# Optimization experiments

Measured on AMD Instinct MI355X. Metric: run time of the kernel, lower is better.

Reference implementation:

```python
import jax, jax.numpy as jnp
import numpy as np
from jax import lax

B, C_IN, C_OUT, H, W, K = 32, 128, 256, 56, 56, 3
STRIDE, PAD = 1, 1
LAMBDA_C, LAMBDA_A = 0.0, 1.0  # adaptive_weights=False defaults


def setup_inputs() -> dict:
    key = jax.random.key(0)
    k1, k2, k3 = jax.random.split(key, 3)
    x = jax.random.normal(k1, (B, C_IN, H, W), dtype=jnp.float32)
    weight = jax.random.normal(k2, (C_OUT, C_IN, K, K), dtype=jnp.float32) * 0.05
    bias = jax.random.normal(k3, (C_OUT,), dtype=jnp.float32) * 0.05
    return {"x": x, "weight": weight, "bias": bias}


def reference(x, weight, bias):
    # For each k x k patch X and kernel slice Kc (per in-channel):
    #   sum(X@Kc) = sum_{a,c} X[a,c] * rowsum(Kc)[c]   (depends on patch column index)
    #   sum(Kc@X) = sum_{c,b} X[c,b] * colsum(Kc)[c]   (depends on patch row index)
    # So lambda_c*(XK-KX).sum() + lambda_a*(XK+KX).sum() summed over in-channels is
    # exactly a conv2d with the effective kernel below.
    krow = weight.sum(axis=3)  # [O, I, k]  rowsum: sum over last kernel axis
    kcol = weight.sum(axis=2)  # [O, I, k]  colsum: sum over first kernel axis
    # W_eff[o,i,r,s] = (la+lc)*krow[o,i,s] + (la-lc)*kcol[o,i,r]
    w_eff = (LAMBDA_A + LAMBDA_C) * krow[:, :, None, :] \
          + (LAMBDA_A - LAMBDA_C) * kcol[:, :, :, None]
    y = lax.conv_general_dilated(
        x, w_eff,
        window_strides=(STRIDE, STRIDE),
        padding=[(PAD, PAD), (PAD, PAD)],
        dimension_numbers=("NCHW", "OIHW", "NCHW"),
    )
    return y + bias[None, :, None, None]
```

## Files before the change

kernel.cpp:

```cpp
#include <hip/hip_runtime.h>
#include <hip/hip_fp16.h>
#include <stdint.h>

typedef unsigned short u16;
typedef _Float16 half8 __attribute__((ext_vector_type(8)));
typedef float floatx4 __attribute__((ext_vector_type(4)));

#define B_N 32
#define CI  128
#define CO  256
#define HH  56
#define WW  56
#define HP  58
#define WP  58

static const size_t XP_OFF = 590080;
static const size_t XP_SZ  = (size_t)32 * 58 * 7424 * 2;
static const size_t XV_OFF = XP_OFF + XP_SZ;
static const size_t XV_SZ  = (size_t)32 * 56 * 7424 * 2;
static const size_t XH_OFF = XV_OFF + XV_SZ;
static const size_t XH_SZ  = (size_t)32 * 58 * 7168 * 2;
static const size_t WS_NEED = XH_OFF + XH_SZ + 1024;

__device__ __forceinline__ float bf2f(u16 u) {
  union { uint32_t i; float f; } c; c.i = ((uint32_t)u) << 16; return c.f;
}
__device__ __forceinline__ u16 f2bf(float f) {
  union { float f; uint32_t i; } c; c.f = f;
  uint32_t u = c.i;
  u += 0x7fffu + ((u >> 16) & 1u);
  return (u16)(u >> 16);
}
__device__ __forceinline__ u16 f2h16(float f) {
  __half h = __float2half_rn(f);
  return *reinterpret_cast<u16*>(&h);
}
__device__ __forceinline__ uint32_t pack2h(float a, float b) {
  __half2 h = __floats2half2_rn(a, b);
  return *reinterpret_cast<uint32_t*>(&h);
}
__device__ __forceinline__ int4 add3(int4 a, int4 b, int4 c) {
  __half2* pa = (__half2*)&a; __half2* pb = (__half2*)&b; __half2* pc = (__half2*)&c;
  int4 r; __half2* pr = (__half2*)&r;
#pragma unroll
  for (int i = 0; i < 4; ++i) pr[i] = __hadd2(__hadd2(pa[i], pb[i]), pc[i]);
  return r;
}

__device__ __forceinline__ bool detect_bf16(const void* __restrict__ bias) {
  int lane = threadIdx.x & 63;
  float a = fabsf(bf2f(((const u16*)bias)[lane]));
  bool plausible = (a >= 1e-5f) && (a <= 0.5f);
  unsigned long long m = __ballot(plausible);
  return __popcll(m) >= 50;
}

__global__ __launch_bounds__(256) void k_prep(const void* __restrict__ xsrc,
                                              const void* __restrict__ wsrc,
                                              u16* __restrict__ xp,
                                              u16* __restrict__ wb,
                                              const void* __restrict__ bias) {
  const int hp = blockIdx.x, b = blockIdx.y, tid = threadIdx.x;
  if (hp == HP) {
    const bool isbf = detect_bf16(bias);
#pragma unroll 1
    for (int sub = 0; sub < 4; ++sub) {
      int t = (b * 4 + sub) * 256 + tid;
      float v[9];
      if (isbf) {
        const u16* p = (const u16*)wsrc + (size_t)t * 9;
#pragma unroll
        for (int j = 0; j < 9; ++j) v[j] = bf2f(p[j]);
      } else {
        const float* p = (const float*)wsrc + (size_t)t * 9;
#pragma unroll
        for (int j = 0; j < 9; ++j) v[j] = p[j];
      }
      float rowsum[3] = { v[0]+v[1]+v[2], v[3]+v[4]+v[5], v[6]+v[7]+v[8] };
      float colsum[3] = { v[0]+v[3]+v[6], v[1]+v[4]+v[7], v[2]+v[5]+v[8] };
      const int o = t >> 7, i = t & 127;
      const int osub = o >> 4, lo = o & 15;
      const int ic = i >> 5, q = (i >> 3) & 3, j = i & 7;
#pragma unroll
      for (int s = 0; s < 3; ++s) {
        int k = s * 4 + ic;
        wb[((size_t)(k * 16 + osub) * 64 + q * 16 + lo) * 8 + j] = f2h16(rowsum[s]);
      }
#pragma unroll
      for (int r = 0; r < 3; ++r) {
        int k = 12 + r * 4 + ic;
        wb[((size_t)(k * 16 + osub) * 64 + q * 16 + lo) * 8 + j] = f2h16(colsum[r]);
      }
    }
    return;
  }
  __shared__ uint32_t tile32[CI * 29];
  u16* dst = xp + (size_t)(b * HP + hp) * (16 * WP * 8);
  if (hp == 0 || hp == HP - 1) {
    int4 z = {0, 0, 0, 0};
    for (int c = tid; c < 928; c += 256) *(int4*)(dst + c * 8) = z;
    return;
  }
  const bool isbf = detect_bf16(bias);
  const int h = hp - 1;
  if (isbf) {
    const uint32_t* xr = (const uint32_t*)xsrc;
    for (int c = tid; c < CI * 28; c += 256) {
      int i = c / 28, wp = c - i * 28;
      uint32_t p2 = xr[((size_t)(b * CI + i) * HH + h) * 28 + wp];
      tile32[i * 29 + wp] = pack2h(bf2f((u16)p2), bf2f((u16)(p2 >> 16)));
    }
  } else {
    const float4* xr = (const float4*)xsrc;
    for (int c = tid; c < CI * 14; c += 256) {
      int i = c / 14, f4 = c - i * 14;
      float4 v = xr[((size_t)(b * CI + i) * HH + h) * 14 + f4];
      tile32[i * 29 + 2 * f4]     = pack2h(v.x, v.y);
      tile32[i * 29 + 2 * f4 + 1] = pack2h(v.z, v.w);
    }
  }
  __syncthreads();
  const u16* t16 = (const u16*)tile32;
  uint32_t* dw = (uint32_t*)dst;
  for (int c = tid; c < 16 * 56 * 4; c += 256) {
    int g = c / 224, rem = c - g * 224, w = rem >> 2, jj = rem & 3;
    int i0 = g * 8 + jj * 2;
    uint32_t lo16 = t16[i0 * 58 + w], hi16 = t16[(i0 + 1) * 58 + w];
    dw[(g * 58 + (w + 1)) * 4 + jj] = lo16 | (hi16 << 16);
  }
  if (tid < 128) {
    int g = tid >> 3, k = tid & 7, wb_ = (k >> 2) * 57, jj = k & 3;
    dw[(g * 58 + wb_) * 4 + jj] = 0;
  }
}

__global__ __launch_bounds__(256) void k_box(const u16* __restrict__ xp,
                                             u16* __restrict__ xv,
                                             u16* __restrict__ xh) {
  const int u = blockIdx.x, b = blockIdx.y, tid = threadIdx.x;
  const int4* r0 = (const int4*)(xp + (size_t)(b * HP + u) * 7424);
  int4* hd = (int4*)(xh + (size_t)(b * HP + u) * 7168);
  for (int c = tid; c < 16 * 56; c += 256) {
    int g = c / 56, w = c - g * 56;
    const int4* s = r0 + g * 58 + w;
    hd[c] = add3(s[0], s[1], s[2]);
  }
  if (u < HH) {
    int4* vd = (int4*)(xv + (size_t)(b * HH + u) * 7424);
    const int4 *r1 = r0 + 928, *r2 = r0 + 1856;
    for (int c = tid; c < 928; c += 256) vd[c] = add3(r0[c], r1[c], r2[c]);
  }
}

#define GSTRIDE 472
#define RSTRIDE (16 * 472)

#define ALOAD(BUF, K)                                                       \
  {                                                                         \
    const u16* ap = wb + ((size_t)((K)*16 + osubbase) << 9) + lane * 8;     \
    af[BUF][0] = *(const half8*)ap;                                         \
    af[BUF][1] = *(const half8*)(ap + 512);                                 \
    af[BUF][2] = *(const half8*)(ap + 1024);                                \
    af[BUF][3] = *(const half8*)(ap + 1536);                                \
  }
#define BLOAD(BUF, K)                                                       \
  {                                                                         \
    int ic_ = (K)&3;                                                        \
    int t_, co_;                                                            \
    if ((K) < 12) { t_ = 2 * rp;                    co_ = (lo + ((K) >> 2)) * 8; } \
    else          { t_ = 4 + 2 * rp + (((K)-12) >> 2); co_ = lo * 8; }      \
    const u16* bp = Bs + ((t_ * 16 + ic_ * 4 + quad) * GSTRIDE) + co_;      \
    bfr[BUF][0] = *(const half8*)bp;                                        \
    bfr[BUF][1] = *(const half8*)(bp + 128);                                \
    bfr[BUF][2] = *(const half8*)(bp + 256);                                \
    bfr[BUF][3] = *(const half8*)(bp + 384);                                \
    bfr[BUF][4] = *(const half8*)(bp + RSTRIDE);                            \
    bfr[BUF][5] = *(const half8*)(bp + RSTRIDE + 128);                      \
    bfr[BUF][6] = *(const half8*)(bp + RSTRIDE + 256);                      \
    bfr[BUF][7] = *(const half8*)(bp + RSTRIDE + 384);                      \
  }
#define MSTEP(BUF)                                                          \
  _Pragma("unroll") for (int m = 0; m < 4; ++m)                             \
      _Pragma("unroll") for (int n = 0; n < 8; ++n) acc[m][n] =             \
          __builtin_amdgcn_mfma_f32_16x16x32_f16(af[BUF][m], bfr[BUF][n],   \
                                                 acc[m][n], 0, 0, 0);

__global__ __launch_bounds__(512, 2) void k_gemm(const u16* __restrict__ wb,
                                                 const u16* __restrict__ xp,
                                                 const void* __restrict__ bias,
                                                 void* __restrict__ outv) {
  __shared__ u16 Bs[10 * RSTRIDE + 64];
  const int lin = blockIdx.y * (HH / 4) + blockIdx.x;
  const int swz = (lin & 7) * (448 / 8) + (lin >> 3);
  const int b = swz / (HH / 4);
  const int p0 = 4 * (swz - b * (HH / 4));
  const int tid = threadIdx.x;
  const int wv = tid >> 6, lane = tid & 63;
  const int lo = lane & 15, quad = lane >> 4;
  const int aq = wv & 3, rp = wv >> 2;
  const int osubbase = aq * 4;

  {
    const u16* xb = xp + (size_t)(b * HP) * 7424;
    for (int c = tid; c < 4 * 928; c += 512) {
      int t = c / 928, rem = c - t * 928;
      const int4* src = (const int4*)(xb + (size_t)(p0 + t) * 7424) + rem;
      int g = rem / 58, w = rem - g * 58;
      *(int4*)(Bs + (size_t)((t * 16 + g) * 59 + w) * 8) =
          add3(src[0], src[928], src[1856]);
    }
    for (int c = tid; c < 6 * 896; c += 512) {
      int u = c / 896, rem = c - u * 896;
      int g = rem / 56, w = rem - g * 56;
      const int4* src = (const int4*)(xb + (size_t)(p0 + u) * 7424) + g * 58 + w;
      *(int4*)(Bs + (size_t)(((4 + u) * 16 + g) * 59 + w) * 8) =
          add3(src[0], src[1], src[2]);
    }
    if (tid < 192) {
      int u = tid / 32, rem = tid - u * 32, g = rem >> 1, w = 56 + (rem & 1);
      *(int4*)(Bs + (size_t)(((4 + u) * 16 + g) * 59 + w) * 8) = (int4){0, 0, 0, 0};
    }
  }
  __syncthreads();

  floatx4 acc[4][8];
#pragma unroll
  for (int m = 0; m < 4; ++m)
#pragma unroll
    for (int n = 0; n < 8; ++n) acc[m][n] = (floatx4){0.f, 0.f, 0.f, 0.f};

  half8 af[2][4], bfr[2][8];
  ALOAD(0, 0); BLOAD(0, 0);
#pragma unroll 1
  for (int k = 0; k < 24; k += 2) {
    ALOAD(1, k + 1); BLOAD(1, k + 1);
    MSTEP(0);
    if (k + 2 < 24) { ALOAD(0, k + 2); BLOAD(0, k + 2); }
    MSTEP(1);
  }

  const bool isbf = detect_bf16(bias);
  const int prow = p0 + 2 * rp;
  if (isbf) {
    u16* out = (u16*)outv;
    const u16* bs = (const u16*)bias;
#pragma unroll
    for (int m = 0; m < 4; ++m)
#pragma unroll
      for (int v = 0; v < 4; ++v) {
        const int o = aq * 64 + m * 16 + quad * 4 + v;
        const float bv = bf2f(bs[o]);
        size_t base = ((size_t)(b * CO + o) * HH + prow) * WW;
#pragma unroll
        for (int n = 0; n < 8; ++n) {
          const int q = (n & 3) * 16 + lo;
          if (q < WW) out[base + (n >> 2) * WW + q] = f2bf(acc[m][n][v] + bv);
        }
      }
  } else {
    float* out = (float*)outv;
    const float* bs = (const float*)bias;
#pragma unroll
    for (int m = 0; m < 4; ++m)
#pragma unroll
      for (int v = 0; v < 4; ++v) {
        const int o = aq * 64 + m * 16 + quad * 4 + v;
        const float bv = bs[o];
        size_t base = ((size_t)(b * CO + o) * HH + prow) * WW;
#pragma unroll
        for (int n = 0; n < 8; ++n) {
          const int q = (n & 3) * 16 + lo;
          if (q < WW) out[base + (n >> 2) * WW + q] = acc[m][n][v] + bv;
        }
      }
  }
}

#define ALOAD_D(BUF, K)                                                     \
  {                                                                         \
    const u16* ap = wb + ((size_t)((K)*16 + osubbase) << 9) + lane * 8;     \
    af[BUF][0] = *(const half8*)ap;                                         \
    af[BUF][1] = *(const half8*)(ap + 512);                                 \
    af[BUF][2] = *(const half8*)(ap + 1024);                                \
    af[BUF][3] = *(const half8*)(ap + 1536);                                \
  }
#define BLOAD_D(BUF, K)                                                     \
  {                                                                         \
    const int g_ = ((K)&3) * 4 + quad;                                      \
    const u16* bp; size_t rstr;                                             \
    if ((K) < 12) {                                                         \
      bp = xv + ((size_t)((b * HH + p0) * 16 + g_)) * 464 + (lo + ((K) >> 2)) * 8; \
      rstr = 7424;                                                          \
    } else {                                                                \
      bp = xh + ((size_t)((b * HP + p0 + (((K)-12) >> 2)) * 16 + g_)) * 448 + lo * 8; \
      rstr = 7168;                                                          \
    }                                                                       \
    bfr[BUF][0] = *(const half8*)bp;                                        \
    bfr[BUF][1] = *(const half8*)(bp + 128);                                \
    bfr[BUF][2] = *(const half8*)(bp + 256);                                \
    bfr[BUF][3] = *(const half8*)(bp + 384);                                \
    bfr[BUF][4] = *(const half8*)(bp + rstr);                               \
    bfr[BUF][5] = *(const half8*)(bp + rstr + 128);                         \
    bfr[BUF][6] = *(const half8*)(bp + rstr + 256);                         \
    bfr[BUF][7] = *(const half8*)(bp + rstr + 384);                         \
  }

__global__ __launch_bounds__(256, 2) void k_gemm_d(const u16* __restrict__ wb,
                                                   const u16* __restrict__ xv,
                                                   const u16* __restrict__ xh,
                                                   const void* __restrict__ bias,
                                                   void* __restrict__ outv) {
  const int lin = blockIdx.y * (HH / 2) + blockIdx.x;
  const int swz = (lin & 7) * 112 + (lin >> 3);
  const int b = swz / (HH / 2);
  const int p0 = 2 * (swz - b * (HH / 2));
  const int tid = threadIdx.x;
  const int wv = tid >> 6, lane = tid & 63;
  const int lo = lane & 15, quad = lane >> 4;
  const int osubbase = wv * 4;

  floatx4 acc[4][8];
#pragma unroll
  for (int m = 0; m < 4; ++m)
#pragma unroll
    for (int n = 0; n < 8; ++n) acc[m][n] = (floatx4){0.f, 0.f, 0.f, 0.f};

  half8 af[2][4], bfr[2][8];
  ALOAD_D(0, 0); BLOAD_D(0, 0);
#pragma unroll 1
  for (int k = 0; k < 24; k += 2) {
    ALOAD_D(1, k + 1); BLOAD_D(1, k + 1);
    MSTEP(0);
    if (k + 2 < 24) { ALOAD_D(0, k + 2); BLOAD_D(0, k + 2); }
    MSTEP(1);
  }

  const bool isbf = detect_bf16(bias);
  if (isbf) {
    u16* out = (u16*)outv;
    const u16* bs = (const u16*)bias;
#pragma unroll
    for (int m = 0; m < 4; ++m)
#pragma unroll
      for (int v = 0; v < 4; ++v) {
        const int o = wv * 64 + m * 16 + quad * 4 + v;
        const float bv = bf2f(bs[o]);
        size_t base = ((size_t)(b * CO + o) * HH + p0) * WW;
#pragma unroll
        for (int n = 0; n < 8; ++n) {
          const int q = (n & 3) * 16 + lo;
          if (q < WW) out[base + (n >> 2) * WW + q] = f2bf(acc[m][n][v] + bv);
        }
      }
  } else {
    float* out = (float*)outv;
    const float* bs = (const float*)bias;
#pragma unroll
    for (int m = 0; m < 4; ++m)
#pragma unroll
      for (int v = 0; v < 4; ++v) {
        const int o = wv * 64 + m * 16 + quad * 4 + v;
        const float bv = bs[o];
        size_t base = ((size_t)(b * CO + o) * HH + p0) * WW;
#pragma unroll
        for (int n = 0; n < 8; ++n) {
          const int q = (n & 3) * 16 + lo;
          if (q < WW) out[base + (n >> 2) * WW + q] = acc[m][n][v] + bv;
        }
      }
  }
}

extern "C" void kernel_launch(void* const* d_in, const int* in_sizes, int n_in,
                              void* d_out, int out_size, void* d_ws, size_t ws_size,
                              hipStream_t stream) {
  const void* x    = d_in[0];
  const void* w    = d_in[1];
  const void* bias = d_in[2];
  uint8_t* ws = (uint8_t*)d_ws;
  u16* wb = (u16*)ws;
  u16* xp = (u16*)(ws + XP_OFF);

  k_prep<<<dim3(HP + 1, B_N), 256, 0, stream>>>(x, w, xp, wb, bias);
  if (ws_size >= WS_NEED) {
    u16* xv = (u16*)(ws + XV_OFF);
    u16* xh = (u16*)(ws + XH_OFF);
    k_box<<<dim3(HP, B_N), 256, 0, stream>>>(xp, xv, xh);
    k_gemm_d<<<dim3(HH / 2, B_N), 256, 0, stream>>>(wb, xv, xh, bias, d_out);
  } else {
    k_gemm<<<dim3(HH / 4, B_N), 512, 0, stream>>>(wb, xp, bias, d_out);
  }
}
```

Before: 222.5 us.

## Fuse vertical box-sum into GEMM via shared memory, drop xv buffer

Stops writing the vertically summed tensor xv to global memory in the box kernel. The GEMM kernel now computes the vertical 3-row sums for its two output rows directly from the padded input and stages them in shared memory, then reads B fragments from LDS for the first 12 k-steps. The horizontal-sum path still reads xh from global memory. This removes one large global write and read pass, at the cost of extra LDS use and a sync at kernel start.

Result: faster. 204.1 us (-8.3%).

```diff
diff --git a/kernel.cpp b/kernel.cpp
--- a/kernel.cpp
+++ b/kernel.cpp
@@ -135,7 +135,6 @@
 }
 
 __global__ __launch_bounds__(256) void k_box(const u16* __restrict__ xp,
-                                             u16* __restrict__ xv,
                                              u16* __restrict__ xh) {
   const int u = blockIdx.x, b = blockIdx.y, tid = threadIdx.x;
   const int4* r0 = (const int4*)(xp + (size_t)(b * HP + u) * 7424);
@@ -145,11 +144,6 @@
     const int4* s = r0 + g * 58 + w;
     hd[c] = add3(s[0], s[1], s[2]);
   }
-  if (u < HH) {
-    int4* vd = (int4*)(xv + (size_t)(b * HH + u) * 7424);
-    const int4 *r1 = r0 + 928, *r2 = r0 + 1856;
-    for (int c = tid; c < 928; c += 256) vd[c] = add3(r0[c], r1[c], r2[c]);
-  }
 }
 
 #define GSTRIDE 472
@@ -163,6 +157,12 @@
     af[BUF][2] = *(const half8*)(ap + 1024);                                \
     af[BUF][3] = *(const half8*)(ap + 1536);                                \
   }
+#define MSTEP(BUF)                                                          \
+  _Pragma("unroll") for (int m = 0; m < 4; ++m)                             \
+      _Pragma("unroll") for (int n = 0; n < 8; ++n) acc[m][n] =             \
+          __builtin_amdgcn_mfma_f32_16x16x32_f16(af[BUF][m], bfr[BUF][n],   \
+                                                 acc[m][n], 0, 0, 0);
+
 #define BLOAD(BUF, K)                                                       \
   {                                                                         \
     int ic_ = (K)&3;                                                        \
@@ -179,11 +179,6 @@
     bfr[BUF][6] = *(const half8*)(bp + RSTRIDE + 256);                      \
     bfr[BUF][7] = *(const half8*)(bp + RSTRIDE + 384);                      \
   }
-#define MSTEP(BUF)                                                          \
-  _Pragma("unroll") for (int m = 0; m < 4; ++m)                             \
-      _Pragma("unroll") for (int n = 0; n < 8; ++n) acc[m][n] =             \
-          __builtin_amdgcn_mfma_f32_16x16x32_f16(af[BUF][m], bfr[BUF][n],   \
-                                                 acc[m][n], 0, 0, 0);
 
 __global__ __launch_bounds__(512, 2) void k_gemm(const u16* __restrict__ wb,
                                                  const u16* __restrict__ xp,
@@ -276,23 +271,15 @@
   }
 }
 
-#define ALOAD_D(BUF, K)                                                     \
+#define BLOAD_H(BUF, K)                                                     \
   {                                                                         \
-    const u16* ap = wb + ((size_t)((K)*16 + osubbase) << 9) + lane * 8;     \
-    af[BUF][0] = *(const half8*)ap;                                         \
-    af[BUF][1] = *(const half8*)(ap + 512);                                 \
-    af[BUF][2] = *(const half8*)(ap + 1024);                                \
-    af[BUF][3] = *(const half8*)(ap + 1536);                                \
-  }
-#define BLOAD_D(BUF, K)                                                     \
-  {                                                                         \
-    const int g_ = ((K)&3) * 4 + quad;                                      \
+    const int ic_ = (K)&3;                                                  \
     const u16* bp; size_t rstr;                                             \
     if ((K) < 12) {                                                         \
-      bp = xv + ((size_t)((b * HH + p0) * 16 + g_)) * 464 + (lo + ((K) >> 2)) * 8; \
-      rstr = 7424;                                                          \
+      bp = Bs + ((ic_ * 4 + quad) * GSTRIDE) + (lo + ((K) >> 2)) * 8;       \
+      rstr = RSTRIDE;                                                       \
     } else {                                                                \
-      bp = xh + ((size_t)((b * HP + p0 + (((K)-12) >> 2)) * 16 + g_)) * 448 + lo * 8; \
+      bp = xh + ((size_t)((b * HP + p0 + (((K)-12) >> 2)) * 16 + ic_ * 4 + quad)) * 448 + lo * 8; \
       rstr = 7168;                                                          \
     }                                                                       \
     bfr[BUF][0] = *(const half8*)bp;                                        \
@@ -300,16 +287,17 @@
     bfr[BUF][2] = *(const half8*)(bp + 256);                                \
     bfr[BUF][3] = *(const half8*)(bp + 384);                                \
     bfr[BUF][4] = *(const half8*)(bp + rstr);                               \
-    bfr[BUF][5] = *(const half8*)(bp + rstr + 128);                         \
-    bfr[BUF][6] = *(const half8*)(bp + rstr + 256);                         \
-    bfr[BUF][7] = *(const half8*)(bp + rstr + 384);                         \
-  }
-
-__global__ __launch_bounds__(256, 2) void k_gemm_d(const u16* __restrict__ wb,
-                                                   const u16* __restrict__ xv,
+    bfr[BUF][5] = *(const half8*)(bp + rstr + 128);                        \
+    bfr[BUF][6] = *(const half8*)(bp + rstr + 256);                        \
+    bfr[BUF][7] = *(const half8*)(bp + rstr + 384);                        \
+  }
+
+__global__ __launch_bounds__(256, 2) void k_gemm_h(const u16* __restrict__ wb,
+                                                   const u16* __restrict__ xp,
                                                    const u16* __restrict__ xh,
                                                    const void* __restrict__ bias,
                                                    void* __restrict__ outv) {
+  __shared__ u16 Bs[2 * RSTRIDE + 64];
   const int lin = blockIdx.y * (HH / 2) + blockIdx.x;
   const int swz = (lin & 7) * 112 + (lin >> 3);
   const int b = swz / (HH / 2);
@@ -319,6 +307,20 @@
   const int lo = lane & 15, quad = lane >> 4;
   const int osubbase = wv * 4;
 
+  {
+    const u16* xb = xp + (size_t)(b * HP) * 7424;
+    for (int c = tid; c < 2 * 928; c += 256) {
+      int t = c >> 9 >= 1 ? c / 928 : 0;
+      t = c / 928;
+      int rem = c - t * 928;
+      const int4* src = (const int4*)(xb + (size_t)(p0 + t) * 7424) + rem;
+      int g = rem / 58, w = rem - g * 58;
+      *(int4*)(Bs + (size_t)((t * 16 + g) * 59 + w) * 8) =
+          add3(src[0], src[928], src[1856]);
+    }
+  }
+  __syncthreads();
+
   floatx4 acc[4][8];
 #pragma unroll
   for (int m = 0; m < 4; ++m)
@@ -326,12 +328,12 @@
     for (int n = 0; n < 8; ++n) acc[m][n] = (floatx4){0.f, 0.f, 0.f, 0.f};
 
   half8 af[2][4], bfr[2][8];
-  ALOAD_D(0, 0); BLOAD_D(0, 0);
+  ALOAD(0, 0); BLOAD_H(0, 0);
 #pragma unroll 1
   for (int k = 0; k < 24; k += 2) {
-    ALOAD_D(1, k + 1); BLOAD_D(1, k + 1);
+    ALOAD(1, k + 1); BLOAD_H(1, k + 1);
     MSTEP(0);
-    if (k + 2 < 24) { ALOAD_D(0, k + 2); BLOAD_D(0, k + 2); }
+    if (k + 2 < 24) { ALOAD(0, k + 2); BLOAD_H(0, k + 2); }
     MSTEP(1);
   }
 
@@ -383,10 +385,9 @@
 
   k_prep<<<dim3(HP + 1, B_N), 256, 0, stream>>>(x, w, xp, wb, bias);
   if (ws_size >= WS_NEED) {
-    u16* xv = (u16*)(ws + XV_OFF);
     u16* xh = (u16*)(ws + XH_OFF);
-    k_box<<<dim3(HP, B_N), 256, 0, stream>>>(xp, xv, xh);
-    k_gemm_d<<<dim3(HH / 2, B_N), 256, 0, stream>>>(wb, xv, xh, bias, d_out);
+    k_box<<<dim3(HP, B_N), 256, 0, stream>>>(xp, xh);
+    k_gemm_h<<<dim3(HH / 2, B_N), 256, 0, stream>>>(wb, xp, xh, bias, d_out);
   } else {
     k_gemm<<<dim3(HH / 4, B_N), 512, 0, stream>>>(wb, xp, bias, d_out);
   }
```

## Fuse box filtering into prep and GEMM, drop separate box kernel

Applied to the files above, without the earlier changes.

Removes the k_box kernel and the xv buffer. The horizontal 3-tap sum is now computed in k_prep from the shared-memory tile. The vertical 3-row sum is built inside the GEMM kernel into LDS from xp. The GEMM is restructured to one output row per block (4x4 MFMA tiles instead of 4x8) with occupancy hint 3, which cuts a launch and a global round trip. The cost is redundant vertical summing per block, less register reuse per block, and an LDS staging sync.

New measurement: 203.5 us. -8.5%, faster.

```diff
diff --git a/kernel.cpp b/kernel.cpp
--- a/kernel.cpp
+++ b/kernel.cpp
@@ -16,9 +16,7 @@
 
 static const size_t XP_OFF = 590080;
 static const size_t XP_SZ  = (size_t)32 * 58 * 7424 * 2;
-static const size_t XV_OFF = XP_OFF + XP_SZ;
-static const size_t XV_SZ  = (size_t)32 * 56 * 7424 * 2;
-static const size_t XH_OFF = XV_OFF + XV_SZ;
+static const size_t XH_OFF = XP_OFF + XP_SZ;
 static const size_t XH_SZ  = (size_t)32 * 58 * 7168 * 2;
 static const size_t WS_NEED = XH_OFF + XH_SZ + 1024;
 
@@ -58,8 +56,10 @@
 __global__ __launch_bounds__(256) void k_prep(const void* __restrict__ xsrc,
                                               const void* __restrict__ wsrc,
                                               u16* __restrict__ xp,
+                                              u16* __restrict__ xh,
                                               u16* __restrict__ wb,
-                                              const void* __restrict__ bias) {
+                                              const void* __restrict__ bias,
+                                              const int do_xh) {
   const int hp = blockIdx.x, b = blockIdx.y, tid = threadIdx.x;
   if (hp == HP) {
     const bool isbf = detect_bf16(bias);
@@ -95,14 +95,18 @@
     return;
   }
   __shared__ uint32_t tile32[CI * 29];
-  u16* dst = xp + (size_t)(b * HP + hp) * (16 * WP * 8);
+  u16* dst  = xp + (size_t)(b * HP + hp) * (16 * WP * 8);
+  u16* dsth = xh + (size_t)(b * HP + hp) * 7168;
   if (hp == 0 || hp == HP - 1) {
     int4 z = {0, 0, 0, 0};
     for (int c = tid; c < 928; c += 256) *(int4*)(dst + c * 8) = z;
+    if (do_xh)
+      for (int c = tid; c < 896; c += 256) *(int4*)(dsth + c * 8) = z;
     return;
   }
   const bool isbf = detect_bf16(bias);
   const int h = hp - 1;
+  if (tid < 128) tile32[tid * 29 + 28] = 0;
   if (isbf) {
     const uint32_t* xr = (const uint32_t*)xsrc;
     for (int c = tid; c < CI * 28; c += 256) {
@@ -132,23 +136,21 @@
     int g = tid >> 3, k = tid & 7, wb_ = (k >> 2) * 57, jj = k & 3;
     dw[(g * 58 + wb_) * 4 + jj] = 0;
   }
-}
-
-__global__ __launch_bounds__(256) void k_box(const u16* __restrict__ xp,
-                                             u16* __restrict__ xv,
-                                             u16* __restrict__ xh) {
-  const int u = blockIdx.x, b = blockIdx.y, tid = threadIdx.x;
-  const int4* r0 = (const int4*)(xp + (size_t)(b * HP + u) * 7424);
-  int4* hd = (int4*)(xh + (size_t)(b * HP + u) * 7168);
-  for (int c = tid; c < 16 * 56; c += 256) {
-    int g = c / 56, w = c - g * 56;
-    const int4* s = r0 + g * 58 + w;
-    hd[c] = add3(s[0], s[1], s[2]);
-  }
-  if (u < HH) {
-    int4* vd = (int4*)(xv + (size_t)(b * HH + u) * 7424);
-    const int4 *r1 = r0 + 928, *r2 = r0 + 1856;
-    for (int c = tid; c < 928; c += 256) vd[c] = add3(r0[c], r1[c], r2[c]);
+  if (do_xh) {
+    const __half* ha = (const __half*)t16;
+    uint32_t* hw = (uint32_t*)dsth;
+    for (int c = tid; c < 16 * 56 * 4; c += 256) {
+      int g = c / 224, rem = c - g * 224, q = rem >> 2, jj = rem & 3;
+      int r0 = (g * 8 + jj * 2) * 58, r1 = r0 + 58;
+      __half zl = __float2half_rn(0.f);
+      __half s0 = (q ? ha[r0 + q - 1] : zl);
+      __half s1 = (q ? ha[r1 + q - 1] : zl);
+      __half lo = __hadd(__hadd(s0, ha[r0 + q]), ha[r0 + q + 1]);
+      __half hi = __hadd(__hadd(s1, ha[r1 + q]), ha[r1 + q + 1]);
+      hw[(g * 56 + q) * 4 + jj] =
+          (uint32_t)*reinterpret_cast<u16*>(&lo) |
+          ((uint32_t)*reinterpret_cast<u16*>(&hi) << 16);
+    }
   }
 }
 
@@ -276,7 +278,7 @@
   }
 }
 
-#define ALOAD_D(BUF, K)                                                     \
+#define ALOAD_S(BUF, K)                                                     \
   {                                                                         \
     const u16* ap = wb + ((size_t)((K)*16 + osubbase) << 9) + lane * 8;     \
     af[BUF][0] = *(const half8*)ap;                                         \
@@ -284,55 +286,65 @@
     af[BUF][2] = *(const half8*)(ap + 1024);                                \
     af[BUF][3] = *(const half8*)(ap + 1536);                                \
   }
-#define BLOAD_D(BUF, K)                                                     \
+#define BLOAD_S(BUF, K)                                                     \
   {                                                                         \
-    const int g_ = ((K)&3) * 4 + quad;                                      \
-    const u16* bp; size_t rstr;                                             \
+    const int ic_ = (K)&3;                                                  \
+    const u16* bp;                                                          \
     if ((K) < 12) {                                                         \
-      bp = xv + ((size_t)((b * HH + p0) * 16 + g_)) * 464 + (lo + ((K) >> 2)) * 8; \
-      rstr = 7424;                                                          \
+      bp = Bs + ((ic_ * 4 + quad) * GSTRIDE) + (lo + ((K) >> 2)) * 8;       \
     } else {                                                                \
-      bp = xh + ((size_t)((b * HP + p0 + (((K)-12) >> 2)) * 16 + g_)) * 448 + lo * 8; \
-      rstr = 7168;                                                          \
+      bp = xh + ((size_t)((b * HP + p + (((K)-12) >> 2)) * 16 + ic_ * 4 + quad)) * 448 + lo * 8; \
     }                                                                       \
     bfr[BUF][0] = *(const half8*)bp;                                        \
     bfr[BUF][1] = *(const half8*)(bp + 128);                                \
     bfr[BUF][2] = *(const half8*)(bp + 256);                                \
     bfr[BUF][3] = *(const half8*)(bp + 384);                                \
-    bfr[BUF][4] = *(const half8*)(bp + rstr);                               \
-    bfr[BUF][5] = *(const half8*)(bp + rstr + 128);                         \
-    bfr[BUF][6] = *(const half8*)(bp + rstr + 256);                         \
-    bfr[BUF][7] = *(const half8*)(bp + rstr + 384);                         \
-  }
-
-__global__ __launch_bounds__(256, 2) void k_gemm_d(const u16* __restrict__ wb,
-                                                   const u16* __restrict__ xv,
+  }
+#define MSTEP_S(BUF)                                                        \
+  _Pragma("unroll") for (int m = 0; m < 4; ++m)                             \
+      _Pragma("unroll") for (int n = 0; n < 4; ++n) acc[m][n] =             \
+          __builtin_amdgcn_mfma_f32_16x16x32_f16(af[BUF][m], bfr[BUF][n],   \
+                                                 acc[m][n], 0, 0, 0);
+
+__global__ __launch_bounds__(256, 3) void k_gemm_s(const u16* __restrict__ wb,
+                                                   const u16* __restrict__ xp,
                                                    const u16* __restrict__ xh,
                                                    const void* __restrict__ bias,
                                                    void* __restrict__ outv) {
-  const int lin = blockIdx.y * (HH / 2) + blockIdx.x;
-  const int swz = (lin & 7) * 112 + (lin >> 3);
-  const int b = swz / (HH / 2);
-  const int p0 = 2 * (swz - b * (HH / 2));
+  __shared__ u16 Bs[RSTRIDE + 128];
+  const int lin = blockIdx.y * HH + blockIdx.x;
+  const int swz = (lin & 7) * (1792 / 8) + (lin >> 3);
+  const int b = swz / HH;
+  const int p = swz - b * HH;
   const int tid = threadIdx.x;
   const int wv = tid >> 6, lane = tid & 63;
   const int lo = lane & 15, quad = lane >> 4;
   const int osubbase = wv * 4;
 
-  floatx4 acc[4][8];
+  {
+    const u16* xb = xp + (size_t)(b * HP + p) * 7424;
+    for (int c = tid; c < 928; c += 256) {
+      const int4* src = (const int4*)xb + c;
+      int g = c / 58, w = c - g * 58;
+      *(int4*)(Bs + (size_t)(g * 59 + w) * 8) = add3(src[0], src[928], src[1856]);
+    }
+  }
+  __syncthreads();
+
+  floatx4 acc[4][4];
 #pragma unroll
   for (int m = 0; m < 4; ++m)
 #pragma unroll
-    for (int n = 0; n < 8; ++n) acc[m][n] = (floatx4){0.f, 0.f, 0.f, 0.f};
-
-  half8 af[2][4], bfr[2][8];
-  ALOAD_D(0, 0); BLOAD_D(0, 0);
+    for (int n = 0; n < 4; ++n) acc[m][n] = (floatx4){0.f, 0.f, 0.f, 0.f};
+
+  half8 af[2][4], bfr[2][4];
+  ALOAD_S(0, 0); BLOAD_S(0, 0);
 #pragma unroll 1
   for (int k = 0; k < 24; k += 2) {
-    ALOAD_D(1, k + 1); BLOAD_D(1, k + 1);
-    MSTEP(0);
-    if (k + 2 < 24) { ALOAD_D(0, k + 2); BLOAD_D(0, k + 2); }
-    MSTEP(1);
+    ALOAD_S(1, k + 1); BLOAD_S(1, k + 1);
+    MSTEP_S(0);
+    if (k + 2 < 24) { ALOAD_S(0, k + 2); BLOAD_S(0, k + 2); }
+    MSTEP_S(1);
   }
 
   const bool isbf = detect_bf16(bias);
@@ -345,11 +357,11 @@
       for (int v = 0; v < 4; ++v) {
         const int o = wv * 64 + m * 16 + quad * 4 + v;
         const float bv = bf2f(bs[o]);
-        size_t base = ((size_t)(b * CO + o) * HH + p0) * WW;
-#pragma unroll
-        for (int n = 0; n < 8; ++n) {
-          const int q = (n & 3) * 16 + lo;
-          if (q < WW) out[base + (n >> 2) * WW + q] = f2bf(acc[m][n][v] + bv);
+        size_t base = ((size_t)(b * CO + o) * HH + p) * WW;
+#pragma unroll
+        for (int n = 0; n < 4; ++n) {
+          const int q = n * 16 + lo;
+          if (q < WW) out[base + q] = f2bf(acc[m][n][v] + bv);
         }
       }
   } else {
@@ -361,11 +373,11 @@
       for (int v = 0; v < 4; ++v) {
         const int o = wv * 64 + m * 16 + quad * 4 + v;
         const float bv = bs[o];
-        size_t base = ((size_t)(b * CO + o) * HH + p0) * WW;
-#pragma unroll
-        for (int n = 0; n < 8; ++n) {
-          const int q = (n & 3) * 16 + lo;
-          if (q < WW) out[base + (n >> 2) * WW + q] = acc[m][n][v] + bv;
+        size_t base = ((size_t)(b * CO + o) * HH + p) * WW;
+#pragma unroll
+        for (int n = 0; n < 4; ++n) {
+          const int q = n * 16 + lo;
+          if (q < WW) out[base + q] = acc[m][n][v] + bv;
         }
       }
   }
@@ -380,13 +392,12 @@
   uint8_t* ws = (uint8_t*)d_ws;
   u16* wb = (u16*)ws;
   u16* xp = (u16*)(ws + XP_OFF);
-
-  k_prep<<<dim3(HP + 1, B_N), 256, 0, stream>>>(x, w, xp, wb, bias);
-  if (ws_size >= WS_NEED) {
-    u16* xv = (u16*)(ws + XV_OFF);
-    u16* xh = (u16*)(ws + XH_OFF);
-    k_box<<<dim3(HP, B_N), 256, 0, stream>>>(xp, xv, xh);
-    k_gemm_d<<<dim3(HH / 2, B_N), 256, 0, stream>>>(wb, xv, xh, bias, d_out);
+  u16* xh = (u16*)(ws + XH_OFF);
+  const int ext = (ws_size >= WS_NEED) ? 1 : 0;
+
+  k_prep<<<dim3(HP + 1, B_N), 256, 0, stream>>>(x, w, xp, xh, wb, bias, ext);
+  if (ext) {
+    k_gemm_s<<<dim3(HH, B_N), 256, 0, stream>>>(wb, xp, xh, bias, d_out);
   } else {
     k_gemm<<<dim3(HH / 4, B_N), 512, 0, stream>>>(wb, xp, bias, d_out);
   }
```
